# Optimization experiments

Measured on AMD Instinct MI355X. Metric: run time of the kernel, lower is better.

The kernel has to match this reference:

```python
import jax, jax.numpy as jnp
import numpy as np

N = 100000   # nodes
E = 600000   # edges
DIN = 128
H = 128
DOUT = 64
EPS = 1e-5   # BatchNorm1d default eps


def setup_inputs() -> dict:
    key = jax.random.key(0)
    ks = jax.random.split(key, 16)
    w = lambda k, shape: jax.random.normal(k, shape, jnp.float32) * 0.05
    return {
        "x": jax.random.normal(ks[0], (N, DIN), jnp.float32),
        "edge_index": jax.random.randint(ks[1], (2, E), 0, N),
        # layer 1: SAGEConv(DIN -> H)  (lin_l on aggregated neighbors w/ bias, lin_r on root)
        "Wl1": w(ks[2], (DIN, H)), "bl1": jnp.zeros((H,), jnp.float32), "Wr1": w(ks[3], (DIN, H)),
        "g1": jnp.ones((H,), jnp.float32), "be1": jnp.zeros((H,), jnp.float32),
        "rm1": jax.random.normal(ks[4], (H,), jnp.float32) * 0.1,
        "rv1": jax.random.uniform(ks[5], (H,), jnp.float32, 0.5, 1.5),
        # layer 2: SAGEConv(H -> H)
        "Wl2": w(ks[6], (H, H)), "bl2": jnp.zeros((H,), jnp.float32), "Wr2": w(ks[7], (H, H)),
        "g2": jnp.ones((H,), jnp.float32), "be2": jnp.zeros((H,), jnp.float32),
        "rm2": jax.random.normal(ks[8], (H,), jnp.float32) * 0.1,
        "rv2": jax.random.uniform(ks[9], (H,), jnp.float32, 0.5, 1.5),
        # layer 3: SAGEConv(H -> DOUT), no BN/ReLU after
        "Wl3": w(ks[10], (H, DOUT)), "bl3": jnp.zeros((DOUT,), jnp.float32), "Wr3": w(ks[11], (H, DOUT)),
    }


def _sage_conv(x, src, dst, Wl, bl, Wr):
    # mean-aggregate source features at targets, then lin_l(agg) + b + lin_r(x)
    agg = jax.ops.segment_sum(x[src], dst, num_segments=N)          # [N, d]
    deg = jax.ops.segment_sum(jnp.ones((src.shape[0],), x.dtype), dst, num_segments=N)
    agg = agg / jnp.maximum(deg, 1.0)[:, None]
    return agg @ Wl + bl + x @ Wr


def _bn_eval(h, g, b, rm, rv):
    return (h - rm) * (g * jax.lax.rsqrt(rv + EPS)) + b


def reference(x, edge_index, Wl1, bl1, Wr1, g1, be1, rm1, rv1,
              Wl2, bl2, Wr2, g2, be2, rm2, rv2, Wl3, bl3, Wr3):
    src, dst = edge_index[0], edge_index[1]
    h = jax.nn.relu(_bn_eval(_sage_conv(x, src, dst, Wl1, bl1, Wr1), g1, be1, rm1, rv1))
    h = jax.nn.relu(_bn_eval(_sage_conv(h, src, dst, Wl2, bl2, Wr2), g2, be2, rm2, rv2))
    return _sage_conv(h, src, dst, Wl3, bl3, Wr3)   # [N, DOUT]
```

## Files before the change

kernel.cpp:

```cpp
#include <hip/hip_runtime.h>

#define CAP 48

typedef short  s8v  __attribute__((ext_vector_type(8)));
typedef float  f4v  __attribute__((ext_vector_type(4)));

__device__ __forceinline__ unsigned short f2bf(float f) {
    unsigned u = __float_as_uint(f);
    u += 0x7FFFu + ((u >> 16) & 1u);
    return (unsigned short)(u >> 16);
}
__device__ __forceinline__ float bflo(unsigned v) { return __uint_as_float(v << 16); }
__device__ __forceinline__ float bfhi(unsigned v) { return __uint_as_float(v & 0xffff0000u); }

#define ACC8(v)  do { a[0]+=bflo((v).x); a[1]+=bfhi((v).x); a[2]+=bflo((v).y); a[3]+=bfhi((v).y); \
                      a[4]+=bflo((v).z); a[5]+=bfhi((v).z); a[6]+=bflo((v).w); a[7]+=bfhi((v).w); } while(0)

__global__ __launch_bounds__(256) void k_bucket(const int* __restrict__ src, const int* __restrict__ dst,
                                                int E, int* __restrict__ cnt, int* __restrict__ bucket) {
    int e = blockIdx.x * 256 + threadIdx.x;
    if (e < E) {
        int d = dst[e];
        int slot = atomicAdd(&cnt[d], 1);
        if (slot < CAP) bucket[(size_t)d * CAP + slot] = src[e];
    }
}

__global__ __launch_bounds__(256) void k_prepack(const float* W0, const float* W1, const float* W2,
                                                 const float* W3, const float* W4, const float* W5,
                                                 unsigned short* P0, unsigned short* P1, unsigned short* P2,
                                                 unsigned short* P3, unsigned short* P4, unsigned short* P5,
                                                 const float* g1, const float* be1, const float* rm1, const float* rv1, const float* bl1,
                                                 const float* g2, const float* be2, const float* rm2, const float* rv2, const float* bl2,
                                                 float* P,
                                                 unsigned short* xb, unsigned short* hb, unsigned short* hb2,
                                                 unsigned short* t3b, int N) {
    if (blockIdx.y == 6) {
        if (blockIdx.x == 0) {
            int i = threadIdx.x;
            if (i < 128) {
                float s1 = g1[i] * rsqrtf(rv1[i] + 1e-5f);
                P[i]       = s1;
                P[128 + i] = (bl1[i] - rm1[i]) * s1 + be1[i];
                float s2 = g2[i] * rsqrtf(rv2[i] + 1e-5f);
                P[256 + i] = s2;
                P[384 + i] = (bl2[i] - rm2[i]) * s2 + be2[i];
                xb [(size_t)N * 128 + i] = 0;
                hb [(size_t)N * 128 + i] = 0;
                hb2[(size_t)N * 128 + i] = 0;
                if (i < 64) t3b[(size_t)N * 64 + i] = 0;
            }
        }
        return;
    }
    const float* W; unsigned short* Pk; int JD;
    switch (blockIdx.y) {
        case 0: W = W0; Pk = P0; JD = 128; break;
        case 1: W = W1; Pk = P1; JD = 128; break;
        case 2: W = W2; Pk = P2; JD = 128; break;
        case 3: W = W3; Pk = P3; JD = 128; break;
        case 4: W = W4; Pk = P4; JD = 64;  break;
        default:W = W5; Pk = P5; JD = 64;  break;
    }
    int o = blockIdx.x * 256 + threadIdx.x;
    if (o >= 128 * JD) return;
    int j    = o & 7;
    int lane = (o >> 3) & 63;
    int t    = o >> 9;
    int nt   = t % (JD / 16);
    int kt   = t / (JD / 16);
    int k = kt * 32 + (lane >> 4) * 8 + j;
    int n = nt * 16 + (lane & 15);
    Pk[o] = f2bf(W[(size_t)k * JD + n]);
}

__global__ __launch_bounds__(256) void k_cvt(const float* __restrict__ in, unsigned short* __restrict__ out, int n4) {
    int i = blockIdx.x * 256 + threadIdx.x;
    if (i < n4) {
        float4 v = ((const float4*)in)[i];
        ushort4 o;
        o.x = f2bf(v.x); o.y = f2bf(v.y); o.z = f2bf(v.z); o.w = f2bf(v.w);
        ((ushort4*)out)[i] = o;
    }
}

template<bool T3>
__global__ __launch_bounds__(256) void k_fused(const unsigned short* __restrict__ feat,
                                               const int* __restrict__ cnt, const int* __restrict__ bucket,
                                               const unsigned short* __restrict__ Bl, const unsigned short* __restrict__ Br,
                                               const float* __restrict__ scale, const float* __restrict__ shift,
                                               unsigned short* __restrict__ out,
                                               const unsigned short* __restrict__ W3p, unsigned short* __restrict__ t3,
                                               int n) {
    __shared__ unsigned short sA[32 * 136];
    __shared__ unsigned short sH[T3 ? 32 * 136 : 8];
    const int tid  = threadIdx.x;
    const int wave = tid >> 6;
    const int lane = tid & 63;
    const int nb0  = blockIdx.x * 32;
    if (nb0 >= n) return;

    {
        const int q4   = lane >> 4;
        const int li   = lane & 15;
        const int base = q4 << 4;
        const uint4* inp = (const uint4*)feat;
        int rows[2], cs[2], idxs[2];
        #pragma unroll
        for (int t = 0; t < 2; t++) {
            rows[t] = wave * 8 + t * 4 + q4;
            int node = nb0 + rows[t];
            bool ok = node < n;
            int c = ok ? cnt[node] : 0; if (c > CAP) c = CAP;
            cs[t] = c;
            idxs[t] = (ok && li < c) ? bucket[(size_t)node * CAP + li] : n;
        }
        #pragma unroll
        for (int t = 0; t < 2; t++) {
            const int c = cs[t];
            float a[8] = {0.f, 0.f, 0.f, 0.f, 0.f, 0.f, 0.f, 0.f};
            if (c > 0) {
                #pragma unroll
                for (int u = 0; u < 8; u++) {
                    int idx = __shfl(idxs[t], base + u);
                    uint4 v = inp[(size_t)idx * 16 + li];
                    ACC8(v);
                }
            }
            if (c > 8) {
                #pragma unroll
                for (int u = 8; u < 16; u++) {
                    int idx = __shfl(idxs[t], base + u);
                    uint4 v = inp[(size_t)idx * 16 + li];
                    ACC8(v);
                }
            }
            const int node = nb0 + rows[t];
            for (int s = 16; s < c; s++) {
                int idx = bucket[(size_t)node * CAP + s];
                uint4 v = inp[(size_t)idx * 16 + li];
                ACC8(v);
            }
            if (node < n) {
                float iv = 1.0f / fmaxf((float)c, 1.0f);
                uint4 o;
                o.x = (unsigned)f2bf(a[0] * iv) | ((unsigned)f2bf(a[1] * iv) << 16);
                o.y = (unsigned)f2bf(a[2] * iv) | ((unsigned)f2bf(a[3] * iv) << 16);
                o.z = (unsigned)f2bf(a[4] * iv) | ((unsigned)f2bf(a[5] * iv) << 16);
                o.w = (unsigned)f2bf(a[6] * iv) | ((unsigned)f2bf(a[7] * iv) << 16);
                *(uint4*)(sA + rows[t] * 136 + li * 8) = o;
            }
        }
    }
    __syncthreads();

    const int m = lane & 15;
    const int q = lane >> 4;
    const int nt0 = wave * 2;
    const int rg0 = min(nb0 + m,      n - 1);
    const int rg1 = min(nb0 + 16 + m, n - 1);

    f4v acc[2][2];
    #pragma unroll
    for (int mt = 0; mt < 2; mt++)
        #pragma unroll
        for (int c = 0; c < 2; c++) {
            acc[mt][c][0] = 0.f; acc[mt][c][1] = 0.f; acc[mt][c][2] = 0.f; acc[mt][c][3] = 0.f;
        }

    #pragma unroll
    for (int kt = 0; kt < 4; kt++) {
        const int ko = kt * 32 + q * 8;
        s8v a0 = *(const s8v*)(sA + m * 136 + ko);
        s8v a1 = *(const s8v*)(sA + (16 + m) * 136 + ko);
        s8v a0d = *(const s8v*)(feat + (size_t)rg0 * 128 + ko);
        s8v a1d = *(const s8v*)(feat + (size_t)rg1 * 128 + ko);
        #pragma unroll
        for (int c = 0; c < 2; c++) {
            s8v b  = *(const s8v*)(Bl + ((size_t)(kt * 8 + nt0 + c) * 64 + lane) * 8);
            acc[0][c] = __builtin_amdgcn_mfma_f32_16x16x32_bf16(a0, b, acc[0][c], 0, 0, 0);
            acc[1][c] = __builtin_amdgcn_mfma_f32_16x16x32_bf16(a1, b, acc[1][c], 0, 0, 0);
            s8v b2 = *(const s8v*)(Br + ((size_t)(kt * 8 + nt0 + c) * 64 + lane) * 8);
            acc[0][c] = __builtin_amdgcn_mfma_f32_16x16x32_bf16(a0d, b2, acc[0][c], 0, 0, 0);
            acc[1][c] = __builtin_amdgcn_mfma_f32_16x16x32_bf16(a1d, b2, acc[1][c], 0, 0, 0);
        }
    }

    float scv[2], shv[2];
    #pragma unroll
    for (int c = 0; c < 2; c++) {
        int col = (nt0 + c) * 16 + m;
        scv[c] = scale[col]; shv[c] = shift[col];
    }
    #pragma unroll
    for (int mt = 0; mt < 2; mt++) {
        #pragma unroll
        for (int reg = 0; reg < 4; reg++) {
            int rloc = mt * 16 + q * 4 + reg;
            int row  = nb0 + rloc;
            if (row < n) {
                #pragma unroll
                for (int c = 0; c < 2; c++) {
                    int col = (nt0 + c) * 16 + m;
                    float v = fmaxf(acc[mt][c][reg] * scv[c] + shv[c], 0.f);
                    unsigned short u = f2bf(v);
                    out[(size_t)row * 128 + col] = u;
                    if constexpr (T3) sH[rloc * 136 + col] = u;
                }
            }
        }
    }

    if constexpr (T3) {
        __syncthreads();
        f4v a3c[2];
        #pragma unroll
        for (int mt = 0; mt < 2; mt++) { a3c[mt][0] = 0.f; a3c[mt][1] = 0.f; a3c[mt][2] = 0.f; a3c[mt][3] = 0.f; }
        #pragma unroll
        for (int kt = 0; kt < 4; kt++) {
            const int ko = kt * 32 + q * 8;
            s8v a0 = *(const s8v*)(sH + m * 136 + ko);
            s8v a1 = *(const s8v*)(sH + (16 + m) * 136 + ko);
            s8v b  = *(const s8v*)(W3p + ((size_t)(kt * 4 + wave) * 64 + lane) * 8);
            a3c[0] = __builtin_amdgcn_mfma_f32_16x16x32_bf16(a0, b, a3c[0], 0, 0, 0);
            a3c[1] = __builtin_amdgcn_mfma_f32_16x16x32_bf16(a1, b, a3c[1], 0, 0, 0);
        }
        #pragma unroll
        for (int mt = 0; mt < 2; mt++) {
            #pragma unroll
            for (int reg = 0; reg < 4; reg++) {
                int row = nb0 + mt * 16 + q * 4 + reg;
                if (row < n) t3[(size_t)row * 64 + wave * 16 + m] = f2bf(a3c[mt][reg]);
            }
        }
    }
}

__global__ __launch_bounds__(256) void k_final(const unsigned short* __restrict__ hb2,
                                               const unsigned short* __restrict__ t3,
                                               const int* __restrict__ cnt, const int* __restrict__ bucket,
                                               const unsigned short* __restrict__ Bp, const float* __restrict__ bias,
                                               float* __restrict__ outf, int n) {
    __shared__ float sG[32 * 68];
    const int tid  = threadIdx.x;
    const int wave = tid >> 6;
    const int lane = tid & 63;
    const int nb0  = blockIdx.x * 32;
    if (nb0 >= n) return;

    {
        const int e8   = lane >> 3;
        const int li   = lane & 7;
        const int base = e8 << 3;
        const uint4* inp = (const uint4*)t3;
        const int row  = wave * 8 + e8;
        const int node = nb0 + row;
        const bool ok  = node < n;
        int c = ok ? cnt[node] : 0; if (c > CAP) c = CAP;
        int idx1 = (ok && li < c)     ? bucket[(size_t)node * CAP + li]     : n;
        int idx2 = (ok && li + 8 < c) ? bucket[(size_t)node * CAP + li + 8] : n;
        float a[8] = {0.f, 0.f, 0.f, 0.f, 0.f, 0.f, 0.f, 0.f};
        if (c > 0) {
            #pragma unroll
            for (int u = 0; u < 8; u++) {
                int idx = __shfl(idx1, base + u);
                uint4 v = inp[(size_t)idx * 8 + li];
                ACC8(v);
            }
        }
        if (c > 8) {
            #pragma unroll
            for (int u = 0; u < 8; u++) {
                int idx = __shfl(idx2, base + u);
                uint4 v = inp[(size_t)idx * 8 + li];
                ACC8(v);
            }
        }
        for (int s = 16; s < c; s++) {
            int idx = bucket[(size_t)node * CAP + s];
            uint4 v = inp[(size_t)idx * 8 + li];
            ACC8(v);
        }
        if (ok) {
            float iv = 1.0f / fmaxf((float)c, 1.0f);
            float4 o1; o1.x = a[0] * iv; o1.y = a[1] * iv; o1.z = a[2] * iv; o1.w = a[3] * iv;
            float4 o2; o2.x = a[4] * iv; o2.y = a[5] * iv; o2.z = a[6] * iv; o2.w = a[7] * iv;
            *(float4*)(sG + row * 68 + li * 8)     = o1;
            *(float4*)(sG + row * 68 + li * 8 + 4) = o2;
        }
    }
    __syncthreads();

    const int m = lane & 15;
    const int q = lane >> 4;
    const int rg0 = min(nb0 + m,      n - 1);
    const int rg1 = min(nb0 + 16 + m, n - 1);

    f4v acc[2];
    #pragma unroll
    for (int mt = 0; mt < 2; mt++) { acc[mt][0] = 0.f; acc[mt][1] = 0.f; acc[mt][2] = 0.f; acc[mt][3] = 0.f; }

    #pragma unroll
    for (int kt = 0; kt < 4; kt++) {
        const int ko = kt * 32 + q * 8;
        s8v a0 = *(const s8v*)(hb2 + (size_t)rg0 * 128 + ko);
        s8v a1 = *(const s8v*)(hb2 + (size_t)rg1 * 128 + ko);
        s8v b  = *(const s8v*)(Bp + ((size_t)(kt * 4 + wave) * 64 + lane) * 8);
        acc[0] = __builtin_amdgcn_mfma_f32_16x16x32_bf16(a0, b, acc[0], 0, 0, 0);
        acc[1] = __builtin_amdgcn_mfma_f32_16x16x32_bf16(a1, b, acc[1], 0, 0, 0);
    }

    const int col = wave * 16 + m;
    const float bv = bias[col];
    #pragma unroll
    for (int mt = 0; mt < 2; mt++) {
        #pragma unroll
        for (int reg = 0; reg < 4; reg++) {
            int rloc = mt * 16 + q * 4 + reg;
            int row  = nb0 + rloc;
            if (row < n) outf[(size_t)row * 64 + col] = acc[mt][reg] + sG[rloc * 68 + col] + bv;
        }
    }
}

extern "C" void kernel_launch(void* const* d_in, const int* in_sizes, int n_in,
                              void* d_out, int out_size, void* d_ws, size_t ws_size,
                              hipStream_t stream) {
    const float* x   = (const float*)d_in[0];
    const int*   ei  = (const int*)d_in[1];
    const float* Wl1 = (const float*)d_in[2];
    const float* bl1 = (const float*)d_in[3];
    const float* Wr1 = (const float*)d_in[4];
    const float* g1  = (const float*)d_in[5];
    const float* be1 = (const float*)d_in[6];
    const float* rm1 = (const float*)d_in[7];
    const float* rv1 = (const float*)d_in[8];
    const float* Wl2 = (const float*)d_in[9];
    const float* bl2 = (const float*)d_in[10];
    const float* Wr2 = (const float*)d_in[11];
    const float* g2  = (const float*)d_in[12];
    const float* be2 = (const float*)d_in[13];
    const float* rm2 = (const float*)d_in[14];
    const float* rv2 = (const float*)d_in[15];
    const float* Wl3 = (const float*)d_in[16];
    const float* bl3 = (const float*)d_in[17];
    const float* Wr3 = (const float*)d_in[18];

    const int N = in_sizes[0] / 128;
    const int E = in_sizes[1] / 2;
    const int* src = ei;
    const int* dst = ei + E;

    char* w = (char*)d_ws;
    auto au = [](size_t v) { return (v + 1023) & ~(size_t)1023; };
    size_t off = 0;
    int*            cnt    = (int*)(w + off);            off += au((size_t)N * 4);
    int*            bucket = (int*)(w + off);            off += au((size_t)N * CAP * 4);
    unsigned short* xb     = (unsigned short*)(w + off); off += au((size_t)(N + 1) * 128 * 2);
    unsigned short* hb     = (unsigned short*)(w + off); off += au((size_t)(N + 1) * 128 * 2);
    unsigned short* hb2    = (unsigned short*)(w + off); off += au((size_t)(N + 1) * 128 * 2);
    unsigned short* t3b    = (unsigned short*)(w + off); off += au((size_t)(N + 1) * 64 * 2);
    unsigned short* Wp[6];
    Wp[0] = (unsigned short*)(w + off); off += au(128 * 128 * 2);
    Wp[1] = (unsigned short*)(w + off); off += au(128 * 128 * 2);
    Wp[2] = (unsigned short*)(w + off); off += au(128 * 128 * 2);
    Wp[3] = (unsigned short*)(w + off); off += au(128 * 128 * 2);
    Wp[4] = (unsigned short*)(w + off); off += au(128 * 64 * 2);
    Wp[5] = (unsigned short*)(w + off); off += au(128 * 64 * 2);
    float* P = (float*)(w + off); off += 2048;
    (void)ws_size; (void)n_in;

    hipMemsetAsync(cnt, 0, (size_t)N * 4, stream);
    k_bucket<<<(E + 255) / 256, 256, 0, stream>>>(src, dst, E, cnt, bucket);
    dim3 pg(64, 7);
    k_prepack<<<pg, 256, 0, stream>>>(Wl1, Wr1, Wl2, Wr2, Wl3, Wr3,
                                      Wp[0], Wp[1], Wp[2], Wp[3], Wp[4], Wp[5],
                                      g1, be1, rm1, rv1, bl1, g2, be2, rm2, rv2, bl2, P,
                                      xb, hb, hb2, t3b, N);
    k_cvt<<<((N * 128 / 4) + 255) / 256, 256, 0, stream>>>(x, xb, N * 128 / 4);

    const int grid = (N + 31) / 32;

    k_fused<false><<<grid, 256, 0, stream>>>(xb, cnt, bucket, Wp[0], Wp[1],
                                             P, P + 128, hb, nullptr, nullptr, N);
    k_fused<true><<<grid, 256, 0, stream>>>(hb, cnt, bucket, Wp[2], Wp[3],
                                            P + 256, P + 384, hb2, Wp[4], t3b, N);
    k_final<<<grid, 256, 0, stream>>>(hb2, t3b, cnt, bucket, Wp[5], bl3, (float*)d_out, N);
}
```

Measured before the change: 297.0 us.

## Merge prep kernels into one launch and make fused kernels grid-stride over tiles

The bucket, conversion and weight-prepack kernels become a single launch that splits work by block-index ranges, which removes two kernel launches and their gaps. The three per-layer kernels now loop over 32-node units with a grid-stride loop at half the previous grid size, so each block handles about two tiles. This cuts block scheduling overhead but lowers the number of blocks available to hide gather latency, and it needs an extra __syncthreads per iteration for shared-memory reuse.

```diff
diff --git a/kernel.cpp b/kernel.cpp
--- a/kernel.cpp
+++ b/kernel.cpp
@@ -13,48 +13,64 @@
 __device__ __forceinline__ float bflo(unsigned v) { return __uint_as_float(v << 16); }
 __device__ __forceinline__ float bfhi(unsigned v) { return __uint_as_float(v & 0xffff0000u); }
 
-#define ACC8(v)  do { a[0]+=bflo((v).x); a[1]+=bfhi((v).x); a[2]+=bflo((v).y); a[3]+=bfhi((v).y); \
-                      a[4]+=bflo((v).z); a[5]+=bfhi((v).z); a[6]+=bflo((v).w); a[7]+=bfhi((v).w); } while(0)
-
-__global__ __launch_bounds__(256) void k_bucket(const int* __restrict__ src, const int* __restrict__ dst,
-                                                int E, int* __restrict__ cnt, int* __restrict__ bucket) {
-    int e = blockIdx.x * 256 + threadIdx.x;
-    if (e < E) {
-        int d = dst[e];
-        int slot = atomicAdd(&cnt[d], 1);
-        if (slot < CAP) bucket[(size_t)d * CAP + slot] = src[e];
-    }
-}
-
-__global__ __launch_bounds__(256) void k_prepack(const float* W0, const float* W1, const float* W2,
-                                                 const float* W3, const float* W4, const float* W5,
-                                                 unsigned short* P0, unsigned short* P1, unsigned short* P2,
-                                                 unsigned short* P3, unsigned short* P4, unsigned short* P5,
-                                                 const float* g1, const float* be1, const float* rm1, const float* rv1, const float* bl1,
-                                                 const float* g2, const float* be2, const float* rm2, const float* rv2, const float* bl2,
-                                                 float* P,
-                                                 unsigned short* xb, unsigned short* hb, unsigned short* hb2,
-                                                 unsigned short* t3b, int N) {
-    if (blockIdx.y == 6) {
-        if (blockIdx.x == 0) {
-            int i = threadIdx.x;
-            if (i < 128) {
-                float s1 = g1[i] * rsqrtf(rv1[i] + 1e-5f);
-                P[i]       = s1;
-                P[128 + i] = (bl1[i] - rm1[i]) * s1 + be1[i];
-                float s2 = g2[i] * rsqrtf(rv2[i] + 1e-5f);
-                P[256 + i] = s2;
-                P[384 + i] = (bl2[i] - rm2[i]) * s2 + be2[i];
-                xb [(size_t)N * 128 + i] = 0;
-                hb [(size_t)N * 128 + i] = 0;
-                hb2[(size_t)N * 128 + i] = 0;
-                if (i < 64) t3b[(size_t)N * 64 + i] = 0;
-            }
+#define ACC8(A_, v) do { (A_)[0]+=bflo((v).x); (A_)[1]+=bfhi((v).x); (A_)[2]+=bflo((v).y); (A_)[3]+=bfhi((v).y); \
+                         (A_)[4]+=bflo((v).z); (A_)[5]+=bfhi((v).z); (A_)[6]+=bflo((v).w); (A_)[7]+=bfhi((v).w); } while(0)
+
+__global__ __launch_bounds__(256) void k_prep(const int* __restrict__ src, const int* __restrict__ dst, int E,
+                                              int* __restrict__ cnt, int* __restrict__ bucket,
+                                              const float* __restrict__ x, unsigned short* __restrict__ xb, int n4,
+                                              const float* W0, const float* W1, const float* W2,
+                                              const float* W3, const float* W4, const float* W5,
+                                              unsigned short* P0, unsigned short* P1, unsigned short* P2,
+                                              unsigned short* P3, unsigned short* P4, unsigned short* P5,
+                                              const float* g1, const float* be1, const float* rm1, const float* rv1, const float* bl1,
+                                              const float* g2, const float* be2, const float* rm2, const float* rv2, const float* bl2,
+                                              float* P,
+                                              unsigned short* hb, unsigned short* hb2, unsigned short* t3b, int N,
+                                              int nbBucket, int nbCvt) {
+    int b = blockIdx.x;
+    const int tid = threadIdx.x;
+    if (b < nbBucket) {
+        int e = b * 256 + tid;
+        if (e < E) {
+            int d = dst[e];
+            int slot = atomicAdd(&cnt[d], 1);
+            if (slot < CAP) bucket[(size_t)d * CAP + slot] = src[e];
         }
         return;
     }
+    b -= nbBucket;
+    if (b < nbCvt) {
+        int i = b * 256 + tid;
+        if (i < n4) {
+            float4 v = ((const float4*)x)[i];
+            ushort4 o;
+            o.x = f2bf(v.x); o.y = f2bf(v.y); o.z = f2bf(v.z); o.w = f2bf(v.w);
+            ((ushort4*)xb)[i] = o;
+        }
+        return;
+    }
+    b -= nbCvt;
+    const int px = b & 63;
+    const int py = b >> 6;
+    if (py == 6) {
+        if (px == 0 && tid < 128) {
+            int i = tid;
+            float s1 = g1[i] * rsqrtf(rv1[i] + 1e-5f);
+            P[i]       = s1;
+            P[128 + i] = (bl1[i] - rm1[i]) * s1 + be1[i];
+            float s2 = g2[i] * rsqrtf(rv2[i] + 1e-5f);
+            P[256 + i] = s2;
+            P[384 + i] = (bl2[i] - rm2[i]) * s2 + be2[i];
+            xb [(size_t)N * 128 + i] = 0;
+            hb [(size_t)N * 128 + i] = 0;
+            hb2[(size_t)N * 128 + i] = 0;
+            if (i < 64) t3b[(size_t)N * 64 + i] = 0;
+        }
+        return;
+    }
     const float* W; unsigned short* Pk; int JD;
-    switch (blockIdx.y) {
+    switch (py) {
         case 0: W = W0; Pk = P0; JD = 128; break;
         case 1: W = W1; Pk = P1; JD = 128; break;
         case 2: W = W2; Pk = P2; JD = 128; break;
@@ -62,7 +78,7 @@
         case 4: W = W4; Pk = P4; JD = 64;  break;
         default:W = W5; Pk = P5; JD = 64;  break;
     }
-    int o = blockIdx.x * 256 + threadIdx.x;
+    int o = px * 256 + tid;
     if (o >= 128 * JD) return;
     int j    = o & 7;
     int lane = (o >> 3) & 63;
@@ -70,18 +86,8 @@
     int nt   = t % (JD / 16);
     int kt   = t / (JD / 16);
     int k = kt * 32 + (lane >> 4) * 8 + j;
-    int n = nt * 16 + (lane & 15);
-    Pk[o] = f2bf(W[(size_t)k * JD + n]);
-}
-
-__global__ __launch_bounds__(256) void k_cvt(const float* __restrict__ in, unsigned short* __restrict__ out, int n4) {
-    int i = blockIdx.x * 256 + threadIdx.x;
-    if (i < n4) {
-        float4 v = ((const float4*)in)[i];
-        ushort4 o;
-        o.x = f2bf(v.x); o.y = f2bf(v.y); o.z = f2bf(v.z); o.w = f2bf(v.w);
-        ((ushort4*)out)[i] = o;
-    }
+    int nn = nt * 16 + (lane & 15);
+    Pk[o] = f2bf(W[(size_t)k * JD + nn]);
 }
 
 template<bool T3>
@@ -91,148 +97,151 @@
                                                const float* __restrict__ scale, const float* __restrict__ shift,
                                                unsigned short* __restrict__ out,
                                                const unsigned short* __restrict__ W3p, unsigned short* __restrict__ t3,
-                                               int n) {
+                                               int n, int units) {
     __shared__ unsigned short sA[32 * 136];
     __shared__ unsigned short sH[T3 ? 32 * 136 : 8];
     const int tid  = threadIdx.x;
     const int wave = tid >> 6;
     const int lane = tid & 63;
-    const int nb0  = blockIdx.x * 32;
-    if (nb0 >= n) return;
-
-    {
-        const int q4   = lane >> 4;
-        const int li   = lane & 15;
-        const int base = q4 << 4;
-        const uint4* inp = (const uint4*)feat;
-        int rows[2], cs[2], idxs[2];
-        #pragma unroll
-        for (int t = 0; t < 2; t++) {
-            rows[t] = wave * 8 + t * 4 + q4;
-            int node = nb0 + rows[t];
-            bool ok = node < n;
-            int c = ok ? cnt[node] : 0; if (c > CAP) c = CAP;
-            cs[t] = c;
-            idxs[t] = (ok && li < c) ? bucket[(size_t)node * CAP + li] : n;
-        }
-        #pragma unroll
-        for (int t = 0; t < 2; t++) {
-            const int c = cs[t];
-            float a[8] = {0.f, 0.f, 0.f, 0.f, 0.f, 0.f, 0.f, 0.f};
-            if (c > 0) {
-                #pragma unroll
-                for (int u = 0; u < 8; u++) {
-                    int idx = __shfl(idxs[t], base + u);
+
+    for (int u = blockIdx.x; u < units; u += gridDim.x) {
+        const int nb0 = u * 32;
+
+        {
+            const int q4   = lane >> 4;
+            const int li   = lane & 15;
+            const int base = q4 << 4;
+            const uint4* inp = (const uint4*)feat;
+            int rows[2], cs[2], idxs[2];
+            #pragma unroll
+            for (int t = 0; t < 2; t++) {
+                rows[t] = wave * 8 + t * 4 + q4;
+                int node = nb0 + rows[t];
+                bool ok = node < n;
+                int c = ok ? cnt[node] : 0; if (c > CAP) c = CAP;
+                cs[t] = c;
+                idxs[t] = (ok && li < c) ? bucket[(size_t)node * CAP + li] : n;
+            }
+            #pragma unroll
+            for (int t = 0; t < 2; t++) {
+                const int c = cs[t];
+                float a[8] = {0.f, 0.f, 0.f, 0.f, 0.f, 0.f, 0.f, 0.f};
+                if (c > 0) {
+                    #pragma unroll
+                    for (int uu = 0; uu < 8; uu++) {
+                        int idx = __shfl(idxs[t], base + uu);
+                        uint4 v = inp[(size_t)idx * 16 + li];
+                        ACC8(a, v);
+                    }
+                }
+                if (c > 8) {
+                    #pragma unroll
+                    for (int uu = 8; uu < 16; uu++) {
+                        int idx = __shfl(idxs[t], base + uu);
+                        uint4 v = inp[(size_t)idx * 16 + li];
+                        ACC8(a, v);
+                    }
+                }
+                const int node = nb0 + rows[t];
+                for (int s = 16; s < c; s++) {
+                    int idx = bucket[(size_t)node * CAP + s];
                     uint4 v = inp[(size_t)idx * 16 + li];
-                    ACC8(v);
-                }
-            }
-            if (c > 8) {
-                #pragma unroll
-                for (int u = 8; u < 16; u++) {
-                    int idx = __shfl(idxs[t], base + u);
-                    uint4 v = inp[(size_t)idx * 16 + li];
-                    ACC8(v);
-                }
-            }
-            const int node = nb0 + rows[t];
-            for (int s = 16; s < c; s++) {
-                int idx = bucket[(size_t)node * CAP + s];
-                uint4 v = inp[(size_t)idx * 16 + li];
-                ACC8(v);
-            }
-            if (node < n) {
-                float iv = 1.0f / fmaxf((float)c, 1.0f);
-                uint4 o;
-                o.x = (unsigned)f2bf(a[0] * iv) | ((unsigned)f2bf(a[1] * iv) << 16);
-                o.y = (unsigned)f2bf(a[2] * iv) | ((unsigned)f2bf(a[3] * iv) << 16);
-                o.z = (unsigned)f2bf(a[4] * iv) | ((unsigned)f2bf(a[5] * iv) << 16);
-                o.w = (unsigned)f2bf(a[6] * iv) | ((unsigned)f2bf(a[7] * iv) << 16);
-                *(uint4*)(sA + rows[t] * 136 + li * 8) = o;
-            }
-        }
-    }
-    __syncthreads();
-
-    const int m = lane & 15;
-    const int q = lane >> 4;
-    const int nt0 = wave * 2;
-    const int rg0 = min(nb0 + m,      n - 1);
-    const int rg1 = min(nb0 + 16 + m, n - 1);
-
-    f4v acc[2][2];
-    #pragma unroll
-    for (int mt = 0; mt < 2; mt++)
-        #pragma unroll
-        for (int c = 0; c < 2; c++) {
-            acc[mt][c][0] = 0.f; acc[mt][c][1] = 0.f; acc[mt][c][2] = 0.f; acc[mt][c][3] = 0.f;
-        }
-
-    #pragma unroll
-    for (int kt = 0; kt < 4; kt++) {
-        const int ko = kt * 32 + q * 8;
-        s8v a0 = *(const s8v*)(sA + m * 136 + ko);
-        s8v a1 = *(const s8v*)(sA + (16 + m) * 136 + ko);
-        s8v a0d = *(const s8v*)(feat + (size_t)rg0 * 128 + ko);
-        s8v a1d = *(const s8v*)(feat + (size_t)rg1 * 128 + ko);
-        #pragma unroll
-        for (int c = 0; c < 2; c++) {
-            s8v b  = *(const s8v*)(Bl + ((size_t)(kt * 8 + nt0 + c) * 64 + lane) * 8);
-            acc[0][c] = __builtin_amdgcn_mfma_f32_16x16x32_bf16(a0, b, acc[0][c], 0, 0, 0);
-            acc[1][c] = __builtin_amdgcn_mfma_f32_16x16x32_bf16(a1, b, acc[1][c], 0, 0, 0);
-            s8v b2 = *(const s8v*)(Br + ((size_t)(kt * 8 + nt0 + c) * 64 + lane) * 8);
-            acc[0][c] = __builtin_amdgcn_mfma_f32_16x16x32_bf16(a0d, b2, acc[0][c], 0, 0, 0);
-            acc[1][c] = __builtin_amdgcn_mfma_f32_16x16x32_bf16(a1d, b2, acc[1][c], 0, 0, 0);
-        }
-    }
-
-    float scv[2], shv[2];
-    #pragma unroll
-    for (int c = 0; c < 2; c++) {
-        int col = (nt0 + c) * 16 + m;
-        scv[c] = scale[col]; shv[c] = shift[col];
-    }
-    #pragma unroll
-    for (int mt = 0; mt < 2; mt++) {
-        #pragma unroll
-        for (int reg = 0; reg < 4; reg++) {
-            int rloc = mt * 16 + q * 4 + reg;
-            int row  = nb0 + rloc;
-            if (row < n) {
-                #pragma unroll
-                for (int c = 0; c < 2; c++) {
-                    int col = (nt0 + c) * 16 + m;
-                    float v = fmaxf(acc[mt][c][reg] * scv[c] + shv[c], 0.f);
-                    unsigned short u = f2bf(v);
-                    out[(size_t)row * 128 + col] = u;
-                    if constexpr (T3) sH[rloc * 136 + col] = u;
-                }
-            }
-        }
-    }
-
-    if constexpr (T3) {
+                    ACC8(a, v);
+                }
+                if (node < n) {
+                    float iv = 1.0f / fmaxf((float)c, 1.0f);
+                    uint4 o;
+                    o.x = (unsigned)f2bf(a[0] * iv) | ((unsigned)f2bf(a[1] * iv) << 16);
+                    o.y = (unsigned)f2bf(a[2] * iv) | ((unsigned)f2bf(a[3] * iv) << 16);
+                    o.z = (unsigned)f2bf(a[4] * iv) | ((unsigned)f2bf(a[5] * iv) << 16);
+                    o.w = (unsigned)f2bf(a[6] * iv) | ((unsigned)f2bf(a[7] * iv) << 16);
+                    *(uint4*)(sA + rows[t] * 136 + li * 8) = o;
+                }
+            }
+        }
         __syncthreads();
-        f4v a3c[2];
-        #pragma unroll
-        for (int mt = 0; mt < 2; mt++) { a3c[mt][0] = 0.f; a3c[mt][1] = 0.f; a3c[mt][2] = 0.f; a3c[mt][3] = 0.f; }
+
+        const int m = lane & 15;
+        const int q = lane >> 4;
+        const int nt0 = wave * 2;
+        const int rg0 = min(nb0 + m,      n - 1);
+        const int rg1 = min(nb0 + 16 + m, n - 1);
+
+        f4v acc[2][2];
+        #pragma unroll
+        for (int mt = 0; mt < 2; mt++)
+            #pragma unroll
+            for (int c = 0; c < 2; c++) {
+                acc[mt][c][0] = 0.f; acc[mt][c][1] = 0.f; acc[mt][c][2] = 0.f; acc[mt][c][3] = 0.f;
+            }
+
         #pragma unroll
         for (int kt = 0; kt < 4; kt++) {
             const int ko = kt * 32 + q * 8;
-            s8v a0 = *(const s8v*)(sH + m * 136 + ko);
-            s8v a1 = *(const s8v*)(sH + (16 + m) * 136 + ko);
-            s8v b  = *(const s8v*)(W3p + ((size_t)(kt * 4 + wave) * 64 + lane) * 8);
-            a3c[0] = __builtin_amdgcn_mfma_f32_16x16x32_bf16(a0, b, a3c[0], 0, 0, 0);
-            a3c[1] = __builtin_amdgcn_mfma_f32_16x16x32_bf16(a1, b, a3c[1], 0, 0, 0);
+            s8v a0 = *(const s8v*)(sA + m * 136 + ko);
+            s8v a1 = *(const s8v*)(sA + (16 + m) * 136 + ko);
+            s8v a0d = *(const s8v*)(feat + (size_t)rg0 * 128 + ko);
+            s8v a1d = *(const s8v*)(feat + (size_t)rg1 * 128 + ko);
+            #pragma unroll
+            for (int c = 0; c < 2; c++) {
+                s8v b  = *(const s8v*)(Bl + ((size_t)(kt * 8 + nt0 + c) * 64 + lane) * 8);
+                acc[0][c] = __builtin_amdgcn_mfma_f32_16x16x32_bf16(a0, b, acc[0][c], 0, 0, 0);
+                acc[1][c] = __builtin_amdgcn_mfma_f32_16x16x32_bf16(a1, b, acc[1][c], 0, 0, 0);
+                s8v b2 = *(const s8v*)(Br + ((size_t)(kt * 8 + nt0 + c) * 64 + lane) * 8);
+                acc[0][c] = __builtin_amdgcn_mfma_f32_16x16x32_bf16(a0d, b2, acc[0][c], 0, 0, 0);
+                acc[1][c] = __builtin_amdgcn_mfma_f32_16x16x32_bf16(a1d, b2, acc[1][c], 0, 0, 0);
+            }
+        }
+
+        float scv[2], shv[2];
+        #pragma unroll
+        for (int c = 0; c < 2; c++) {
+            int col = (nt0 + c) * 16 + m;
+            scv[c] = scale[col]; shv[c] = shift[col];
         }
         #pragma unroll
         for (int mt = 0; mt < 2; mt++) {
             #pragma unroll
             for (int reg = 0; reg < 4; reg++) {
-                int row = nb0 + mt * 16 + q * 4 + reg;
-                if (row < n) t3[(size_t)row * 64 + wave * 16 + m] = f2bf(a3c[mt][reg]);
-            }
-        }
+                int rloc = mt * 16 + q * 4 + reg;
+                int row  = nb0 + rloc;
+                if (row < n) {
+                    #pragma unroll
+                    for (int c = 0; c < 2; c++) {
+                        int col = (nt0 + c) * 16 + m;
+                        float v = fmaxf(acc[mt][c][reg] * scv[c] + shv[c], 0.f);
+                        unsigned short uq = f2bf(v);
+                        out[(size_t)row * 128 + col] = uq;
+                        if constexpr (T3) sH[rloc * 136 + col] = uq;
+                    }
+                }
+            }
+        }
+
+        if constexpr (T3) {
+            __syncthreads();
+            f4v a3c[2];
+            #pragma unroll
+            for (int mt = 0; mt < 2; mt++) { a3c[mt][0] = 0.f; a3c[mt][1] = 0.f; a3c[mt][2] = 0.f; a3c[mt][3] = 0.f; }
+            #pragma unroll
+            for (int kt = 0; kt < 4; kt++) {
+                const int ko = kt * 32 + q * 8;
+                s8v a0 = *(const s8v*)(sH + m * 136 + ko);
+                s8v a1 = *(const s8v*)(sH + (16 + m) * 136 + ko);
+                s8v b  = *(const s8v*)(W3p + ((size_t)(kt * 4 + wave) * 64 + lane) * 8);
+                a3c[0] = __builtin_amdgcn_mfma_f32_16x16x32_bf16(a0, b, a3c[0], 0, 0, 0);
+                a3c[1] = __builtin_amdgcn_mfma_f32_16x16x32_bf16(a1, b, a3c[1], 0, 0, 0);
+            }
+            #pragma unroll
+            for (int mt = 0; mt < 2; mt++) {
+                #pragma unroll
+                for (int reg = 0; reg < 4; reg++) {
+                    int row = nb0 + mt * 16 + q * 4 + reg;
+                    if (row < n) t3[(size_t)row * 64 + wave * 16 + m] = f2bf(a3c[mt][reg]);
+                }
+            }
+        }
+        __syncthreads();
     }
 }
 
@@ -240,86 +249,89 @@
                                                const unsigned short* __restrict__ t3,
                                                const int* __restrict__ cnt, const int* __restrict__ bucket,
                                                const unsigned short* __restrict__ Bp, const float* __restrict__ bias,
-                                               float* __restrict__ outf, int n) {
+                                               float* __restrict__ outf, int n, int units) {
     __shared__ float sG[32 * 68];
     const int tid  = threadIdx.x;
     const int wave = tid >> 6;
     const int lane = tid & 63;
-    const int nb0  = blockIdx.x * 32;
-    if (nb0 >= n) return;
-
-    {
-        const int e8   = lane >> 3;
-        const int li   = lane & 7;
-        const int base = e8 << 3;
-        const uint4* inp = (const uint4*)t3;
-        const int row  = wave * 8 + e8;
-        const int node = nb0 + row;
-        const bool ok  = node < n;
-        int c = ok ? cnt[node] : 0; if (c > CAP) c = CAP;
-        int idx1 = (ok && li < c)     ? bucket[(size_t)node * CAP + li]     : n;
-        int idx2 = (ok && li + 8 < c) ? bucket[(size_t)node * CAP + li + 8] : n;
-        float a[8] = {0.f, 0.f, 0.f, 0.f, 0.f, 0.f, 0.f, 0.f};
-        if (c > 0) {
-            #pragma unroll
-            for (int u = 0; u < 8; u++) {
-                int idx = __shfl(idx1, base + u);
+
+    for (int u = blockIdx.x; u < units; u += gridDim.x) {
+        const int nb0 = u * 32;
+
+        {
+            const int e8   = lane >> 3;
+            const int li   = lane & 7;
+            const int base = e8 << 3;
+            const uint4* inp = (const uint4*)t3;
+            const int row  = wave * 8 + e8;
+            const int node = nb0 + row;
+            const bool ok  = node < n;
+            int c = ok ? cnt[node] : 0; if (c > CAP) c = CAP;
+            int idx1 = (ok && li < c)     ? bucket[(size_t)node * CAP + li]     : n;
+            int idx2 = (ok && li + 8 < c) ? bucket[(size_t)node * CAP + li + 8] : n;
+            float a[8] = {0.f, 0.f, 0.f, 0.f, 0.f, 0.f, 0.f, 0.f};
+            if (c > 0) {
+                #pragma unroll
+                for (int uu = 0; uu < 8; uu++) {
+                    int idx = __shfl(idx1, base + uu);
+                    uint4 v = inp[(size_t)idx * 8 + li];
+                    ACC8(a, v);
+                }
+            }
+            if (c > 8) {
+                #pragma unroll
+                for (int uu = 0; uu < 8; uu++) {
+                    int idx = __shfl(idx2, base + uu);
+                    uint4 v = inp[(size_t)idx * 8 + li];
+                    ACC8(a, v);
+                }
+            }
+            for (int s = 16; s < c; s++) {
+                int idx = bucket[(size_t)node * CAP + s];
                 uint4 v = inp[(size_t)idx * 8 + li];
-                ACC8(v);
-            }
-        }
-        if (c > 8) {
-            #pragma unroll
-            for (int u = 0; u < 8; u++) {
-                int idx = __shfl(idx2, base + u);
-                uint4 v = inp[(size_t)idx * 8 + li];
-                ACC8(v);
-            }
-        }
-        for (int s = 16; s < c; s++) {
-            int idx = bucket[(size_t)node * CAP + s];
-            uint4 v = inp[(size_t)idx * 8 + li];
-            ACC8(v);
-        }
-        if (ok) {
-            float iv = 1.0f / fmaxf((float)c, 1.0f);
-            float4 o1; o1.x = a[0] * iv; o1.y = a[1] * iv; o1.z = a[2] * iv; o1.w = a[3] * iv;
-            float4 o2; o2.x = a[4] * iv; o2.y = a[5] * iv; o2.z = a[6] * iv; o2.w = a[7] * iv;
-            *(float4*)(sG + row * 68 + li * 8)     = o1;
-            *(float4*)(sG + row * 68 + li * 8 + 4) = o2;
-        }
-    }
-    __syncthreads();
-
-    const int m = lane & 15;
-    const int q = lane >> 4;
-    const int rg0 = min(nb0 + m,      n - 1);
-    const int rg1 = min(nb0 + 16 + m, n - 1);
-
-    f4v acc[2];
-    #pragma unroll
-    for (int mt = 0; mt < 2; mt++) { acc[mt][0] = 0.f; acc[mt][1] = 0.f; acc[mt][2] = 0.f; acc[mt][3] = 0.f; }
-
-    #pragma unroll
-    for (int kt = 0; kt < 4; kt++) {
-        const int ko = kt * 32 + q * 8;
-        s8v a0 = *(const s8v*)(hb2 + (size_t)rg0 * 128 + ko);
-        s8v a1 = *(const s8v*)(hb2 + (size_t)rg1 * 128 + ko);
-        s8v b  = *(const s8v*)(Bp + ((size_t)(kt * 4 + wave) * 64 + lane) * 8);
-        acc[0] = __builtin_amdgcn_mfma_f32_16x16x32_bf16(a0, b, acc[0], 0, 0, 0);
-        acc[1] = __builtin_amdgcn_mfma_f32_16x16x32_bf16(a1, b, acc[1], 0, 0, 0);
-    }
-
-    const int col = wave * 16 + m;
-    const float bv = bias[col];
-    #pragma unroll
-    for (int mt = 0; mt < 2; mt++) {
-        #pragma unroll
-        for (int reg = 0; reg < 4; reg++) {
-            int rloc = mt * 16 + q * 4 + reg;
-            int row  = nb0 + rloc;
-            if (row < n) outf[(size_t)row * 64 + col] = acc[mt][reg] + sG[rloc * 68 + col] + bv;
-        }
+                ACC8(a, v);
+            }
+            if (ok) {
+                float iv = 1.0f / fmaxf((float)c, 1.0f);
+                float4 o1; o1.x = a[0] * iv; o1.y = a[1] * iv; o1.z = a[2] * iv; o1.w = a[3] * iv;
+                float4 o2; o2.x = a[4] * iv; o2.y = a[5] * iv; o2.z = a[6] * iv; o2.w = a[7] * iv;
+                *(float4*)(sG + row * 68 + li * 8)     = o1;
+                *(float4*)(sG + row * 68 + li * 8 + 4) = o2;
+            }
+        }
+        __syncthreads();
+
+        const int m = lane & 15;
+        const int q = lane >> 4;
+        const int rg0 = min(nb0 + m,      n - 1);
+        const int rg1 = min(nb0 + 16 + m, n - 1);
+
+        f4v acc[2];
+        #pragma unroll
+        for (int mt = 0; mt < 2; mt++) { acc[mt][0] = 0.f; acc[mt][1] = 0.f; acc[mt][2] = 0.f; acc[mt][3] = 0.f; }
+
+        #pragma unroll
+        for (int kt = 0; kt < 4; kt++) {
+            const int ko = kt * 32 + q * 8;
+            s8v a0 = *(const s8v*)(hb2 + (size_t)rg0 * 128 + ko);
+            s8v a1 = *(const s8v*)(hb2 + (size_t)rg1 * 128 + ko);
+            s8v b  = *(const s8v*)(Bp + ((size_t)(kt * 4 + wave) * 64 + lane) * 8);
+            acc[0] = __builtin_amdgcn_mfma_f32_16x16x32_bf16(a0, b, acc[0], 0, 0, 0);
+            acc[1] = __builtin_amdgcn_mfma_f32_16x16x32_bf16(a1, b, acc[1], 0, 0, 0);
+        }
+
+        const int col = wave * 16 + m;
+        const float bv = bias[col];
+        #pragma unroll
+        for (int mt = 0; mt < 2; mt++) {
+            #pragma unroll
+            for (int reg = 0; reg < 4; reg++) {
+                int rloc = mt * 16 + q * 4 + reg;
+                int row  = nb0 + rloc;
+                if (row < n) outf[(size_t)row * 64 + col] = acc[mt][reg] + sG[rloc * 68 + col] + bv;
+            }
+        }
+        __syncthreads();
     }
 }
 
@@ -371,19 +383,23 @@
     (void)ws_size; (void)n_in;
 
     hipMemsetAsync(cnt, 0, (size_t)N * 4, stream);
-    k_bucket<<<(E + 255) / 256, 256, 0, stream>>>(src, dst, E, cnt, bucket);
-    dim3 pg(64, 7);
-    k_prepack<<<pg, 256, 0, stream>>>(Wl1, Wr1, Wl2, Wr2, Wl3, Wr3,
-                                      Wp[0], Wp[1], Wp[2], Wp[3], Wp[4], Wp[5],
-                                      g1, be1, rm1, rv1, bl1, g2, be2, rm2, rv2, bl2, P,
-                                      xb, hb, hb2, t3b, N);
-    k_cvt<<<((N * 128 / 4) + 255) / 256, 256, 0, stream>>>(x, xb, N * 128 / 4);
-
-    const int grid = (N + 31) / 32;
+
+    const int n4 = N * 32;
+    const int nbBucket = (E + 255) / 256;
+    const int nbCvt    = (n4 + 255) / 256;
+    k_prep<<<nbBucket + nbCvt + 448, 256, 0, stream>>>(src, dst, E, cnt, bucket,
+                                                       x, xb, n4,
+                                                       Wl1, Wr1, Wl2, Wr2, Wl3, Wr3,
+                                                       Wp[0], Wp[1], Wp[2], Wp[3], Wp[4], Wp[5],
+                                                       g1, be1, rm1, rv1, bl1, g2, be2, rm2, rv2, bl2, P,
+                                                       hb, hb2, t3b, N, nbBucket, nbCvt);
+
+    const int units = (N + 31) / 32;
+    const int grid  = (units + 1) / 2;
 
     k_fused<false><<<grid, 256, 0, stream>>>(xb, cnt, bucket, Wp[0], Wp[1],
-                                             P, P + 128, hb, nullptr, nullptr, N);
+                                             P, P + 128, hb, nullptr, nullptr, N, units);
     k_fused<true><<<grid, 256, 0, stream>>>(hb, cnt, bucket, Wp[2], Wp[3],
-                                            P + 256, P + 384, hb2, Wp[4], t3b, N);
-    k_final<<<grid, 256, 0, stream>>>(hb2, t3b, cnt, bucket, Wp[5], bl3, (float*)d_out, N);
+                                            P + 256, P + 384, hb2, Wp[4], t3b, N, units);
+    k_final<<<grid, 256, 0, stream>>>(hb2, t3b, cnt, bucket, Wp[5], bl3, (float*)d_out, N, units);
 }
```

Result: slower. 305.3 us (+2.8%).
